# Kernel tuning notes

Measured on AMD Instinct MI355X. Metric: run time of the kernel, lower is better.

## Reference

```python
import jax, jax.numpy as jnp
import numpy as np

B, S, I, H = 32, 1024, 1024, 1024

def setup_inputs() -> dict:
    key = jax.random.key(0)
    k1, k2, k3, k4, k5 = jax.random.split(key, 5)
    bound = 1.0 / np.sqrt(I + H)  # nn.Linear default init scale
    return {
        "x": jax.random.normal(k1, (B, S, I), dtype=jnp.float32),
        "h0": jax.random.normal(k2, (1, B, H), dtype=jnp.float32),
        "c0": jax.random.normal(k3, (1, B, H), dtype=jnp.float32),
        "W": jax.random.uniform(k4, (H, I + H), dtype=jnp.float32, minval=-bound, maxval=bound),
        "b": jax.random.uniform(k5, (H,), dtype=jnp.float32, minval=-bound, maxval=bound),
    }

def reference(x, h0, c0, W, b):
    # NOTE: original torch module applies the SAME linear layer to h_x for all
    # four gates, so f_t == i_t == o_t == sigmoid(z) and C_tilde = tanh(z).
    # Concat order is (h, x): W[:, :H] multiplies h, W[:, H:] multiplies x.
    Wh = W[:, :x.shape[-1] if False else h0.shape[-1]]  # [H, H]
    Wx = W[:, h0.shape[-1]:]                            # [H, I]
    h_init = h0[0]  # [B, H]
    c_init = c0[0]  # [B, H]
    # Precompute the input contribution for all timesteps in one big GEMM.
    xz = jnp.einsum('bsi,hi->sbh', x, Wx) + b  # [S, B, H]

    def step(carry, xz_t):
        h, c = carry
        z = h @ Wh.T + xz_t          # [B, H] shared gate pre-activation
        s = jax.nn.sigmoid(z)        # f_t == i_t == o_t
        c_new = s * c + s * jnp.tanh(z)
        h_new = s * jnp.tanh(c_new)
        return (h_new, c_new), h_new

    (hn, cn), outs = jax.lax.scan(step, (h_init, c_init), xz)
    out = jnp.swapaxes(outs, 0, 1)  # [B, S, H]
    return out, hn[None], cn[None]
```

## Files before the change

### kernel.cpp

```cpp
#include <hip/hip_runtime.h>

#define B_ 32
#define S_ 1024
#define H_ 1024
#define NWG 64
#define EXN (32 * 1024)

typedef float f32x4 __attribute__((ext_vector_type(4)));
typedef short bf16x8 __attribute__((ext_vector_type(8)));
typedef unsigned short u16;

__device__ __forceinline__ short f2bf(float f) {
  union { float f; unsigned u; } v; v.f = f;
  unsigned r = v.u + 0x7FFFu + ((v.u >> 16) & 1u);
  return (short)(r >> 16);
}

__device__ __forceinline__ bf16x8 ldg_coh_b8(const u16* p) {
  bf16x8 r;
  asm volatile("global_load_dwordx4 %0, %1, off sc0 sc1"
               : "=v"(r) : "v"(p) : "memory");
  return r;
}
__device__ __forceinline__ void stg_coh_u16(u16* p, u16 v) {
  asm volatile("global_store_short %0, %1, off sc0 sc1"
               :: "v"(p), "v"(v) : "memory");
}

__global__ __launch_bounds__(256) void xz_gemm(
    const float* __restrict__ X, const float* __restrict__ W,
    const float* __restrict__ bias, float* __restrict__ C) {
  __shared__ short As[128][40];
  __shared__ short Bs[128][40];
  const int tid  = threadIdx.x;
  const int lane = tid & 63, wave = tid >> 6;
  const int m0 = blockIdx.y * 128, n0 = blockIdx.x * 128;
  const int wm = (wave >> 1) * 64, wn = (wave & 1) * 64;
  const int jl = lane & 15, kq = lane >> 4;
  const int sr = tid >> 2, skg = (tid & 3) * 8;

  f32x4 zero4 = {0.f, 0.f, 0.f, 0.f};
  f32x4 acc[4][4];
  #pragma unroll
  for (int mi = 0; mi < 4; ++mi)
    #pragma unroll
    for (int ni = 0; ni < 4; ++ni) acc[mi][ni] = zero4;

  for (int k0 = 0; k0 < 1024; k0 += 32) {
    #pragma unroll
    for (int rr = 0; rr < 2; ++rr) {
      int row = sr + rr * 64;
      const float* pa = X + (size_t)(m0 + row) * 1024 + k0 + skg;
      f32x4 a0 = *(const f32x4*)pa;
      f32x4 a1 = *(const f32x4*)(pa + 4);
      bf16x8 pk;
      #pragma unroll
      for (int e = 0; e < 4; ++e) { pk[e] = f2bf(a0[e]); pk[e + 4] = f2bf(a1[e]); }
      *(bf16x8*)&As[row][skg] = pk;
      const float* pb = W + (size_t)(n0 + row) * 2048 + 1024 + k0 + skg;
      f32x4 b0 = *(const f32x4*)pb;
      f32x4 b1 = *(const f32x4*)(pb + 4);
      bf16x8 qk;
      #pragma unroll
      for (int e = 0; e < 4; ++e) { qk[e] = f2bf(b0[e]); qk[e + 4] = f2bf(b1[e]); }
      *(bf16x8*)&Bs[row][skg] = qk;
    }
    __syncthreads();
    bf16x8 af[4], bfv[4];
    #pragma unroll
    for (int mi = 0; mi < 4; ++mi) af[mi] = *(const bf16x8*)&As[wm + mi * 16 + jl][kq * 8];
    #pragma unroll
    for (int ni = 0; ni < 4; ++ni) bfv[ni] = *(const bf16x8*)&Bs[wn + ni * 16 + jl][kq * 8];
    #pragma unroll
    for (int mi = 0; mi < 4; ++mi)
      #pragma unroll
      for (int ni = 0; ni < 4; ++ni)
        acc[mi][ni] = __builtin_amdgcn_mfma_f32_16x16x32_bf16(af[mi], bfv[ni], acc[mi][ni], 0, 0, 0);
    __syncthreads();
  }
  #pragma unroll
  for (int ni = 0; ni < 4; ++ni) {
    int col = n0 + wn + ni * 16 + jl;
    float bv = bias[col];
    #pragma unroll
    for (int mi = 0; mi < 4; ++mi) {
      int rbase = m0 + wm + mi * 16 + kq * 4;
      #pragma unroll
      for (int r = 0; r < 4; ++r)
        C[(size_t)(rbase + r) * 1024 + col] = acc[mi][ni][r] + bv;
    }
  }
}

__global__ __launch_bounds__(512) void lstm_rec(
    const float* __restrict__ W, const float* __restrict__ h0,
    const float* __restrict__ c0, float* __restrict__ out,
    u16* __restrict__ exch, unsigned* __restrict__ flags) {
  __shared__ short Whs[32 * 1024];
  __shared__ float zred[8][2][64][4];
  const int tid  = threadIdx.x;
  const int lane = tid & 63, wave = tid >> 6;
  const int jl = lane & 15, kq = lane >> 4;
  const int bg = blockIdx.x >> 5;
  const int cg = blockIdx.x & 31;

  {
    int j  = tid >> 4;
    int g0 = (tid & 15) * 8;
    const float* wrow = W + (size_t)(cg * 32 + j) * 2048;
    #pragma unroll
    for (int g = 0; g < 8; ++g) {
      int grp = g0 + g;
      const float* p = wrow + grp * 8;
      f32x4 a0 = *(const f32x4*)p;
      f32x4 a1 = *(const f32x4*)(p + 4);
      bf16x8 pk;
      #pragma unroll
      for (int e = 0; e < 4; ++e) { pk[e] = f2bf(a0[e]); pk[e + 4] = f2bf(a1[e]); }
      *(bf16x8*)&Whs[(j * 128 + (grp ^ (j & 7))) * 8] = pk;
    }
  }

  const int bp   = tid >> 5;
  const int cp   = tid & 31;
  const int b    = bg * 16 + bp;
  const int col  = cg * 32 + cp;
  float cst  = c0[b * 1024 + col];
  float hcur = 0.f;
  stg_coh_u16(exch + b * 1024 + col, (u16)f2bf(h0[b * 1024 + col]));
  __syncthreads();
  if (tid == 0)
    __hip_atomic_store(&flags[blockIdx.x * 16], 1u,
                       __ATOMIC_RELAXED, __HIP_MEMORY_SCOPE_AGENT);

  bf16x8 bfr[2][4];
  #pragma unroll
  for (int ct = 0; ct < 2; ++ct)
    #pragma unroll
    for (int kk = 0; kk < 4; ++kk) {
      int j2  = ct * 16 + jl;
      int grp = wave * 16 + kk * 4 + kq;
      bfr[ct][kk] = *(const bf16x8*)&Whs[(j2 * 128 + (grp ^ (j2 & 7))) * 8];
    }

  const int ct_o = cp >> 4;
  const int j16  = cp & 15;
  const int lred = ((bp >> 2) << 4) | j16;
  const int rred = bp & 3;
  const size_t obase = (size_t)b * (S_ * H_) + col;
  const u16* aptr = exch + (size_t)(bg * 16 + jl) * 1024 + wave * 128 + kq * 8;

  for (int t = 0; t < S_; ++t) {
    float xz = out[obase + (size_t)t * H_];

    if (lane < 4) {
      const unsigned* fp = flags + ((bg << 5) | (wave * 4 + lane)) * 16;
      while (__hip_atomic_load(fp, __ATOMIC_RELAXED, __HIP_MEMORY_SCOPE_AGENT)
             < (unsigned)(t + 1))
        __builtin_amdgcn_s_sleep(1);
    }

    const u16* src = aptr + (t & 1) * EXN;
    bf16x8 afr[4];
    #pragma unroll
    for (int kk = 0; kk < 4; ++kk) afr[kk] = ldg_coh_b8(src + kk * 32);
    asm volatile("s_waitcnt vmcnt(0)" ::: "memory");
    __builtin_amdgcn_sched_barrier(0);

    #pragma unroll
    for (int ct = 0; ct < 2; ++ct) {
      f32x4 pacc = {0.f, 0.f, 0.f, 0.f};
      #pragma unroll
      for (int kk = 0; kk < 4; ++kk)
        pacc = __builtin_amdgcn_mfma_f32_16x16x32_bf16(afr[kk], bfr[ct][kk], pacc, 0, 0, 0);
      *(f32x4*)&zred[wave][ct][lane][0] = pacc;
    }
    __syncthreads();

    float z = xz;
    #pragma unroll
    for (int w = 0; w < 8; ++w) z += zred[w][ct_o][lred][rred];
    float sg  = 1.f / (1.f + __expf(-z));
    float e2z = __expf(2.f * z);
    float tz  = 1.f - 2.f / (e2z + 1.f);
    cst  = sg * (cst + tz);
    float e2c = __expf(2.f * cst);
    float tc  = 1.f - 2.f / (e2c + 1.f);
    hcur = sg * tc;
    stg_coh_u16(exch + ((t + 1) & 1) * EXN + b * 1024 + col, (u16)f2bf(hcur));
    __syncthreads();
    if (tid == 0)
      __hip_atomic_store(&flags[blockIdx.x * 16], (unsigned)(t + 2),
                         __ATOMIC_RELAXED, __HIP_MEMORY_SCOPE_AGENT);
    out[obase + (size_t)t * H_] = hcur;
  }

  const size_t OFS = (size_t)B_ * S_ * H_;
  out[OFS + b * 1024 + col] = hcur;
  out[OFS + (size_t)B_ * H_ + b * 1024 + col] = cst;
}

extern "C" void kernel_launch(void* const* d_in, const int* in_sizes, int n_in,
                              void* d_out, int out_size, void* d_ws, size_t ws_size,
                              hipStream_t stream) {
  const float* x    = (const float*)d_in[0];
  const float* h0   = (const float*)d_in[1];
  const float* c0   = (const float*)d_in[2];
  const float* W    = (const float*)d_in[3];
  const float* bias = (const float*)d_in[4];
  float* out = (float*)d_out;

  u16* exch = (u16*)d_ws;
  unsigned* flags = (unsigned*)((char*)d_ws + 2 * EXN * sizeof(u16));
  hipMemsetAsync(flags, 0, NWG * 16 * sizeof(unsigned), stream);

  xz_gemm<<<dim3(8, 256), 256, 0, stream>>>(x, W, bias, out);
  lstm_rec<<<dim3(NWG), 512, 0, stream>>>(W, h0, c0, out, exch, flags);
}
```

Measured before the change: 2.635 ms.

## Replace flag-based inter-block sync with tagged h exchange words

New measurement: 3.437 ms. 30.4% more time.

```diff
diff --git a/kernel.cpp b/kernel.cpp
--- a/kernel.cpp
+++ b/kernel.cpp
@@ -4,10 +4,11 @@
 #define S_ 1024
 #define H_ 1024
 #define NWG 64
-#define EXN (32 * 1024)
+#define EXN32 (32 * 1024)
 
 typedef float f32x4 __attribute__((ext_vector_type(4)));
 typedef short bf16x8 __attribute__((ext_vector_type(8)));
+typedef unsigned int u32x4 __attribute__((ext_vector_type(4)));
 typedef unsigned short u16;
 
 __device__ __forceinline__ short f2bf(float f) {
@@ -16,15 +17,18 @@
   return (short)(r >> 16);
 }
 
-__device__ __forceinline__ bf16x8 ldg_coh_b8(const u16* p) {
-  bf16x8 r;
-  asm volatile("global_load_dwordx4 %0, %1, off sc0 sc1"
-               : "=v"(r) : "v"(p) : "memory");
-  return r;
-}
-__device__ __forceinline__ void stg_coh_u16(u16* p, u16 v) {
-  asm volatile("global_store_short %0, %1, off sc0 sc1"
+__device__ __forceinline__ void stg_coh_u32(unsigned* p, unsigned v) {
+  asm volatile("global_store_dword %0, %1, off sc0 sc1"
                :: "v"(p), "v"(v) : "memory");
+}
+
+__device__ __forceinline__ bf16x8 mk_frag(u32x4 lo, u32x4 hi) {
+  union { unsigned u[4]; bf16x8 v; } c;
+  c.u[0] = (lo[0] >> 16) | (lo[1] & 0xffff0000u);
+  c.u[1] = (lo[2] >> 16) | (lo[3] & 0xffff0000u);
+  c.u[2] = (hi[0] >> 16) | (hi[1] & 0xffff0000u);
+  c.u[3] = (hi[2] >> 16) | (hi[3] & 0xffff0000u);
+  return c.v;
 }
 
 __global__ __launch_bounds__(256) void xz_gemm(
@@ -95,9 +99,9 @@
 __global__ __launch_bounds__(512) void lstm_rec(
     const float* __restrict__ W, const float* __restrict__ h0,
     const float* __restrict__ c0, float* __restrict__ out,
-    u16* __restrict__ exch, unsigned* __restrict__ flags) {
+    unsigned* __restrict__ exch) {
   __shared__ short Whs[32 * 1024];
-  __shared__ float zred[8][2][64][4];
+  __shared__ float zred[2][8][2][64][5];
   const int tid  = threadIdx.x;
   const int lane = tid & 63, wave = tid >> 6;
   const int jl = lane & 15, kq = lane >> 4;
@@ -121,17 +125,15 @@
     }
   }
 
-  const int bp   = tid >> 5;
-  const int cp   = tid & 31;
-  const int b    = bg * 16 + bp;
-  const int col  = cg * 32 + cp;
+  const int bp  = tid >> 5;
+  const int cp  = tid & 31;
+  const int b   = bg * 16 + bp;
+  const int col = cg * 32 + cp;
   float cst  = c0[b * 1024 + col];
   float hcur = 0.f;
-  stg_coh_u16(exch + b * 1024 + col, (u16)f2bf(h0[b * 1024 + col]));
+  stg_coh_u32(exch + b * 1024 + col,
+              ((unsigned)(u16)f2bf(h0[b * 1024 + col]) << 16) | 1u);
   __syncthreads();
-  if (tid == 0)
-    __hip_atomic_store(&flags[blockIdx.x * 16], 1u,
-                       __ATOMIC_RELAXED, __HIP_MEMORY_SCOPE_AGENT);
 
   bf16x8 bfr[2][4];
   #pragma unroll
@@ -148,38 +150,62 @@
   const int lred = ((bp >> 2) << 4) | j16;
   const int rred = bp & 3;
   const size_t obase = (size_t)b * (S_ * H_) + col;
-  const u16* aptr = exch + (size_t)(bg * 16 + jl) * 1024 + wave * 128 + kq * 8;
+  const unsigned* aptr = exch + (size_t)(bg * 16 + jl) * 1024 + wave * 128 + kq * 8;
+
+  float xz = out[obase];
 
   for (int t = 0; t < S_; ++t) {
-    float xz = out[obase + (size_t)t * H_];
-
-    if (lane < 4) {
-      const unsigned* fp = flags + ((bg << 5) | (wave * 4 + lane)) * 16;
-      while (__hip_atomic_load(fp, __ATOMIC_RELAXED, __HIP_MEMORY_SCOPE_AGENT)
-             < (unsigned)(t + 1))
-        __builtin_amdgcn_s_sleep(1);
-    }
-
-    const u16* src = aptr + (t & 1) * EXN;
+    const unsigned* srcb = aptr + (size_t)(t & 1) * EXN32;
+    const unsigned etag  = (unsigned)(t + 1);
+
+    u32x4 L0, L1, L2, L3, L4, L5, L6, L7;
+#define LDC(dst, off) asm volatile( \
+    "global_load_dwordx4 %0, %1, off offset:" off " sc0 sc1" \
+    : "=v"(dst) : "v"(srcb) : "memory")
+    for (;;) {
+      LDC(L0, "0");   LDC(L1, "16");
+      LDC(L2, "128"); LDC(L3, "144");
+      LDC(L4, "256"); LDC(L5, "272");
+      LDC(L6, "384"); LDC(L7, "400");
+      asm volatile("s_waitcnt vmcnt(0)" ::: "memory");
+      __builtin_amdgcn_sched_barrier(0);
+      unsigned acc;
+      acc  = (L0[0] ^ etag) | (L0[1] ^ etag) | (L0[2] ^ etag) | (L0[3] ^ etag);
+      acc |= (L1[0] ^ etag) | (L1[1] ^ etag) | (L1[2] ^ etag) | (L1[3] ^ etag);
+      acc |= (L2[0] ^ etag) | (L2[1] ^ etag) | (L2[2] ^ etag) | (L2[3] ^ etag);
+      acc |= (L3[0] ^ etag) | (L3[1] ^ etag) | (L3[2] ^ etag) | (L3[3] ^ etag);
+      acc |= (L4[0] ^ etag) | (L4[1] ^ etag) | (L4[2] ^ etag) | (L4[3] ^ etag);
+      acc |= (L5[0] ^ etag) | (L5[1] ^ etag) | (L5[2] ^ etag) | (L5[3] ^ etag);
+      acc |= (L6[0] ^ etag) | (L6[1] ^ etag) | (L6[2] ^ etag) | (L6[3] ^ etag);
+      acc |= (L7[0] ^ etag) | (L7[1] ^ etag) | (L7[2] ^ etag) | (L7[3] ^ etag);
+      if (__all((acc & 0xffffu) == 0u)) break;
+    }
+#undef LDC
+
     bf16x8 afr[4];
-    #pragma unroll
-    for (int kk = 0; kk < 4; ++kk) afr[kk] = ldg_coh_b8(src + kk * 32);
-    asm volatile("s_waitcnt vmcnt(0)" ::: "memory");
-    __builtin_amdgcn_sched_barrier(0);
-
+    afr[0] = mk_frag(L0, L1);
+    afr[1] = mk_frag(L2, L3);
+    afr[2] = mk_frag(L4, L5);
+    afr[3] = mk_frag(L6, L7);
     #pragma unroll
     for (int ct = 0; ct < 2; ++ct) {
       f32x4 pacc = {0.f, 0.f, 0.f, 0.f};
       #pragma unroll
       for (int kk = 0; kk < 4; ++kk)
         pacc = __builtin_amdgcn_mfma_f32_16x16x32_bf16(afr[kk], bfr[ct][kk], pacc, 0, 0, 0);
-      *(f32x4*)&zred[wave][ct][lane][0] = pacc;
-    }
+      #pragma unroll
+      for (int r = 0; r < 4; ++r)
+        zred[t & 1][wave][ct][lane][r] = pacc[r];
+    }
+
+    const size_t nxi = obase + (size_t)(t + 1 < S_ ? t + 1 : t) * H_;
+    float xz_next = out[nxi];
+
     __syncthreads();
 
     float z = xz;
     #pragma unroll
-    for (int w = 0; w < 8; ++w) z += zred[w][ct_o][lred][rred];
+    for (int w = 0; w < 8; ++w) z += zred[t & 1][w][ct_o][lred][rred];
     float sg  = 1.f / (1.f + __expf(-z));
     float e2z = __expf(2.f * z);
     float tz  = 1.f - 2.f / (e2z + 1.f);
@@ -187,12 +213,10 @@
     float e2c = __expf(2.f * cst);
     float tc  = 1.f - 2.f / (e2c + 1.f);
     hcur = sg * tc;
-    stg_coh_u16(exch + ((t + 1) & 1) * EXN + b * 1024 + col, (u16)f2bf(hcur));
-    __syncthreads();
-    if (tid == 0)
-      __hip_atomic_store(&flags[blockIdx.x * 16], (unsigned)(t + 2),
-                         __ATOMIC_RELAXED, __HIP_MEMORY_SCOPE_AGENT);
+    stg_coh_u32(exch + (size_t)((t + 1) & 1) * EXN32 + b * 1024 + col,
+                ((unsigned)(u16)f2bf(hcur) << 16) | (unsigned)(t + 2));
     out[obase + (size_t)t * H_] = hcur;
+    xz = xz_next;
   }
 
   const size_t OFS = (size_t)B_ * S_ * H_;
@@ -210,10 +234,9 @@
   const float* bias = (const float*)d_in[4];
   float* out = (float*)d_out;
 
-  u16* exch = (u16*)d_ws;
-  unsigned* flags = (unsigned*)((char*)d_ws + 2 * EXN * sizeof(u16));
-  hipMemsetAsync(flags, 0, NWG * 16 * sizeof(unsigned), stream);
+  unsigned* exch = (unsigned*)d_ws;
+  hipMemsetAsync(exch, 0, 2 * EXN32 * sizeof(unsigned), stream);
 
   xz_gemm<<<dim3(8, 256), 256, 0, stream>>>(x, W, bias, out);
-  lstm_rec<<<dim3(NWG), 512, 0, stream>>>(W, h0, c0, out, exch, flags);
-}
+  lstm_rec<<<dim3(NWG), 512, 0, stream>>>(W, h0, c0, out, exch);
+}
```

## Restructure recurrent kernel to single-wave workgroups holding Wh slice in registers

Applied to the files above, without the earlier changes.

Result: slower. 4.239 ms (+60.9%).

```diff
diff --git a/kernel.cpp b/kernel.cpp
--- a/kernel.cpp
+++ b/kernel.cpp
@@ -3,7 +3,6 @@
 #define B_ 32
 #define S_ 1024
 #define H_ 1024
-#define NWG 64
 #define EXN (32 * 1024)
 
 typedef float f32x4 __attribute__((ext_vector_type(4)));
@@ -16,14 +15,12 @@
   return (short)(r >> 16);
 }
 
-__device__ __forceinline__ bf16x8 ldg_coh_b8(const u16* p) {
-  bf16x8 r;
-  asm volatile("global_load_dwordx4 %0, %1, off sc0 sc1"
-               : "=v"(r) : "v"(p) : "memory");
-  return r;
-}
 __device__ __forceinline__ void stg_coh_u16(u16* p, u16 v) {
   asm volatile("global_store_short %0, %1, off sc0 sc1"
+               :: "v"(p), "v"(v) : "memory");
+}
+__device__ __forceinline__ void stg_coh_u32(unsigned* p, unsigned v) {
+  asm volatile("global_store_dword %0, %1, off sc0 sc1"
                :: "v"(p), "v"(v) : "memory");
 }
 
@@ -92,112 +89,114 @@
   }
 }
 
-__global__ __launch_bounds__(512) void lstm_rec(
+__global__ __launch_bounds__(64) void lstm_rec(
     const float* __restrict__ W, const float* __restrict__ h0,
     const float* __restrict__ c0, float* __restrict__ out,
     u16* __restrict__ exch, unsigned* __restrict__ flags) {
-  __shared__ short Whs[32 * 1024];
-  __shared__ float zred[8][2][64][4];
-  const int tid  = threadIdx.x;
-  const int lane = tid & 63, wave = tid >> 6;
-  const int jl = lane & 15, kq = lane >> 4;
-  const int bg = blockIdx.x >> 5;
-  const int cg = blockIdx.x & 31;
-
+  const int lane = threadIdx.x & 63;
+  const int wg   = blockIdx.x;
+  const int bt   = wg >> 6;
+  const int ct   = wg & 63;
+  const int jl   = lane & 15, kq = lane >> 4;
+
+  bf16x8 Bf[32];
   {
-    int j  = tid >> 4;
-    int g0 = (tid & 15) * 8;
-    const float* wrow = W + (size_t)(cg * 32 + j) * 2048;
-    #pragma unroll
-    for (int g = 0; g < 8; ++g) {
-      int grp = g0 + g;
-      const float* p = wrow + grp * 8;
+    const float* wrow = W + (size_t)(ct * 16 + jl) * 2048;
+    #pragma unroll
+    for (int kk = 0; kk < 32; ++kk) {
+      const float* p = wrow + kk * 32 + kq * 8;
       f32x4 a0 = *(const f32x4*)p;
       f32x4 a1 = *(const f32x4*)(p + 4);
       bf16x8 pk;
       #pragma unroll
       for (int e = 0; e < 4; ++e) { pk[e] = f2bf(a0[e]); pk[e + 4] = f2bf(a1[e]); }
-      *(bf16x8*)&Whs[(j * 128 + (grp ^ (j & 7))) * 8] = pk;
-    }
-  }
-
-  const int bp   = tid >> 5;
-  const int cp   = tid & 31;
-  const int b    = bg * 16 + bp;
-  const int col  = cg * 32 + cp;
-  float cst  = c0[b * 1024 + col];
-  float hcur = 0.f;
-  stg_coh_u16(exch + b * 1024 + col, (u16)f2bf(h0[b * 1024 + col]));
-  __syncthreads();
-  if (tid == 0)
-    __hip_atomic_store(&flags[blockIdx.x * 16], 1u,
-                       __ATOMIC_RELAXED, __HIP_MEMORY_SCOPE_AGENT);
-
-  bf16x8 bfr[2][4];
-  #pragma unroll
-  for (int ct = 0; ct < 2; ++ct)
-    #pragma unroll
-    for (int kk = 0; kk < 4; ++kk) {
-      int j2  = ct * 16 + jl;
-      int grp = wave * 16 + kk * 4 + kq;
-      bfr[ct][kk] = *(const bf16x8*)&Whs[(j2 * 128 + (grp ^ (j2 & 7))) * 8];
-    }
-
-  const int ct_o = cp >> 4;
-  const int j16  = cp & 15;
-  const int lred = ((bp >> 2) << 4) | j16;
-  const int rred = bp & 3;
-  const size_t obase = (size_t)b * (S_ * H_) + col;
-  const u16* aptr = exch + (size_t)(bg * 16 + jl) * 1024 + wave * 128 + kq * 8;
+      Bf[kk] = pk;
+    }
+  }
+
+  const int b0  = bt * 16 + kq * 4;
+  const int col = ct * 16 + jl;
+  float c[4], h[4];
+  #pragma unroll
+  for (int r = 0; r < 4; ++r) {
+    c[r] = c0[(b0 + r) * 1024 + col];
+    h[r] = h0[(b0 + r) * 1024 + col];
+  }
+  #pragma unroll
+  for (int r = 0; r < 4; ++r)
+    stg_coh_u16(exch + (b0 + r) * 1024 + col, (u16)f2bf(h[r]));
+  asm volatile("s_waitcnt vmcnt(0)" ::: "memory");
+  unsigned* myflag = flags + wg;
+  if (lane == 0) stg_coh_u32(myflag, 1u);
+
+  const u16* aB = exch + (size_t)(bt * 16 + jl) * 1024 + kq * 8;
+  const unsigned* fptr = flags + (bt << 6) + lane;
 
   for (int t = 0; t < S_; ++t) {
-    float xz = out[obase + (size_t)t * H_];
-
-    if (lane < 4) {
-      const unsigned* fp = flags + ((bg << 5) | (wave * 4 + lane)) * 16;
-      while (__hip_atomic_load(fp, __ATOMIC_RELAXED, __HIP_MEMORY_SCOPE_AGENT)
-             < (unsigned)(t + 1))
-        __builtin_amdgcn_s_sleep(1);
-    }
-
-    const u16* src = aptr + (t & 1) * EXN;
-    bf16x8 afr[4];
-    #pragma unroll
-    for (int kk = 0; kk < 4; ++kk) afr[kk] = ldg_coh_b8(src + kk * 32);
+    float xz[4];
+    #pragma unroll
+    for (int r = 0; r < 4; ++r)
+      xz[r] = out[((size_t)(b0 + r) * S_ + t) * H_ + col];
+
+    unsigned fv;
+    for (;;) {
+      asm volatile("global_load_dword %0, %1, off sc0 sc1"
+                   : "=v"(fv) : "v"(fptr) : "memory");
+      asm volatile("s_waitcnt vmcnt(0)" ::: "memory");
+      if (__all(fv > (unsigned)t)) break;
+      __builtin_amdgcn_s_sleep(1);
+    }
+    __builtin_amdgcn_sched_barrier(0);
+
+    const u16* src = aB + (size_t)(t & 1) * EXN;
+    bf16x8 A[32];
+#define LDA(K, OFF) asm volatile( \
+    "global_load_dwordx4 %0, %1, off offset:" OFF " sc0 sc1" \
+    : "=v"(A[K]) : "v"(src) : "memory")
+    LDA(0, "0");     LDA(1, "64");    LDA(2, "128");   LDA(3, "192");
+    LDA(4, "256");   LDA(5, "320");   LDA(6, "384");   LDA(7, "448");
+    LDA(8, "512");   LDA(9, "576");   LDA(10, "640");  LDA(11, "704");
+    LDA(12, "768");  LDA(13, "832");  LDA(14, "896");  LDA(15, "960");
+    LDA(16, "1024"); LDA(17, "1088"); LDA(18, "1152"); LDA(19, "1216");
+    LDA(20, "1280"); LDA(21, "1344"); LDA(22, "1408"); LDA(23, "1472");
+    LDA(24, "1536"); LDA(25, "1600"); LDA(26, "1664"); LDA(27, "1728");
+    LDA(28, "1792"); LDA(29, "1856"); LDA(30, "1920"); LDA(31, "1984");
+#undef LDA
     asm volatile("s_waitcnt vmcnt(0)" ::: "memory");
     __builtin_amdgcn_sched_barrier(0);
 
-    #pragma unroll
-    for (int ct = 0; ct < 2; ++ct) {
-      f32x4 pacc = {0.f, 0.f, 0.f, 0.f};
-      #pragma unroll
-      for (int kk = 0; kk < 4; ++kk)
-        pacc = __builtin_amdgcn_mfma_f32_16x16x32_bf16(afr[kk], bfr[ct][kk], pacc, 0, 0, 0);
-      *(f32x4*)&zred[wave][ct][lane][0] = pacc;
-    }
-    __syncthreads();
-
-    float z = xz;
-    #pragma unroll
-    for (int w = 0; w < 8; ++w) z += zred[w][ct_o][lred][rred];
-    float sg  = 1.f / (1.f + __expf(-z));
-    float e2z = __expf(2.f * z);
-    float tz  = 1.f - 2.f / (e2z + 1.f);
-    cst  = sg * (cst + tz);
-    float e2c = __expf(2.f * cst);
-    float tc  = 1.f - 2.f / (e2c + 1.f);
-    hcur = sg * tc;
-    stg_coh_u16(exch + ((t + 1) & 1) * EXN + b * 1024 + col, (u16)f2bf(hcur));
-    __syncthreads();
-    if (tid == 0)
-      __hip_atomic_store(&flags[blockIdx.x * 16], (unsigned)(t + 2),
-                         __ATOMIC_RELAXED, __HIP_MEMORY_SCOPE_AGENT);
-    out[obase + (size_t)t * H_] = hcur;
+    f32x4 acc[4];
+    #pragma unroll
+    for (int a = 0; a < 4; ++a) acc[a] = (f32x4){0.f, 0.f, 0.f, 0.f};
+    #pragma unroll
+    for (int kk = 0; kk < 32; ++kk)
+      acc[kk & 3] = __builtin_amdgcn_mfma_f32_16x16x32_bf16(A[kk], Bf[kk], acc[kk & 3], 0, 0, 0);
+
+    u16* dst = exch + (size_t)((t + 1) & 1) * EXN;
+    #pragma unroll
+    for (int r = 0; r < 4; ++r) {
+      float z  = xz[r] + (acc[0][r] + acc[1][r]) + (acc[2][r] + acc[3][r]);
+      float u  = __expf(-z);
+      float u2 = u * u;
+      float sg = __builtin_amdgcn_rcpf(1.f + u);
+      float tz = (1.f - u2) * __builtin_amdgcn_rcpf(1.f + u2);
+      c[r] = sg * (c[r] + tz);
+      float v  = __expf(-2.f * c[r]);
+      float tc = (1.f - v) * __builtin_amdgcn_rcpf(1.f + v);
+      h[r] = sg * tc;
+      out[((size_t)(b0 + r) * S_ + t) * H_ + col] = h[r];
+      stg_coh_u16(dst + (b0 + r) * 1024 + col, (u16)f2bf(h[r]));
+    }
+    asm volatile("s_waitcnt vmcnt(0)" ::: "memory");
+    if (lane == 0) stg_coh_u32(myflag, (unsigned)(t + 2));
   }
 
   const size_t OFS = (size_t)B_ * S_ * H_;
-  out[OFS + b * 1024 + col] = hcur;
-  out[OFS + (size_t)B_ * H_ + b * 1024 + col] = cst;
+  #pragma unroll
+  for (int r = 0; r < 4; ++r) {
+    out[OFS + (b0 + r) * 1024 + col] = h[r];
+    out[OFS + (size_t)B_ * H_ + (b0 + r) * 1024 + col] = c[r];
+  }
 }
 
 extern "C" void kernel_launch(void* const* d_in, const int* in_sizes, int n_in,
@@ -212,8 +211,8 @@
 
   u16* exch = (u16*)d_ws;
   unsigned* flags = (unsigned*)((char*)d_ws + 2 * EXN * sizeof(u16));
-  hipMemsetAsync(flags, 0, NWG * 16 * sizeof(unsigned), stream);
+  hipMemsetAsync(flags, 0, 128 * sizeof(unsigned), stream);
 
   xz_gemm<<<dim3(8, 256), 256, 0, stream>>>(x, W, bias, out);
-  lstm_rec<<<dim3(NWG), 512, 0, stream>>>(W, h0, c0, out, exch, flags);
-}
+  lstm_rec<<<dim3(128), 64, 0, stream>>>(W, h0, c0, out, exch, flags);
+}
```

## Replace second block barrier with LDS counter publish and lighter coherence flags

Applied to the files above, without the earlier changes.

Measured after the change: 3.017 ms. 1.14x slower.

```diff
diff --git a/kernel.cpp b/kernel.cpp
--- a/kernel.cpp
+++ b/kernel.cpp
@@ -16,15 +16,11 @@
   return (short)(r >> 16);
 }
 
-__device__ __forceinline__ bf16x8 ldg_coh_b8(const u16* p) {
-  bf16x8 r;
-  asm volatile("global_load_dwordx4 %0, %1, off sc0 sc1"
-               : "=v"(r) : "v"(p) : "memory");
-  return r;
-}
 __device__ __forceinline__ void stg_coh_u16(u16* p, u16 v) {
-  asm volatile("global_store_short %0, %1, off sc0 sc1"
-               :: "v"(p), "v"(v) : "memory");
+  asm volatile("global_store_short %0, %1, off sc1" :: "v"(p), "v"(v) : "memory");
+}
+__device__ __forceinline__ void stg_coh_u32(unsigned* p, unsigned v) {
+  asm volatile("global_store_dword %0, %1, off sc1" :: "v"(p), "v"(v) : "memory");
 }
 
 __global__ __launch_bounds__(256) void xz_gemm(
@@ -97,12 +93,15 @@
     const float* __restrict__ c0, float* __restrict__ out,
     u16* __restrict__ exch, unsigned* __restrict__ flags) {
   __shared__ short Whs[32 * 1024];
-  __shared__ float zred[8][2][64][4];
+  __shared__ float zred[2][8][2][64][5];
+  __shared__ unsigned pubcnt[2];
   const int tid  = threadIdx.x;
   const int lane = tid & 63, wave = tid >> 6;
   const int jl = lane & 15, kq = lane >> 4;
   const int bg = blockIdx.x >> 5;
   const int cg = blockIdx.x & 31;
+
+  if (tid < 2) pubcnt[tid] = 0u;
 
   {
     int j  = tid >> 4;
@@ -121,17 +120,16 @@
     }
   }
 
-  const int bp   = tid >> 5;
-  const int cp   = tid & 31;
-  const int b    = bg * 16 + bp;
-  const int col  = cg * 32 + cp;
+  const int bp  = tid >> 5;
+  const int cp  = tid & 31;
+  const int b   = bg * 16 + bp;
+  const int col = cg * 32 + cp;
   float cst  = c0[b * 1024 + col];
   float hcur = 0.f;
   stg_coh_u16(exch + b * 1024 + col, (u16)f2bf(h0[b * 1024 + col]));
   __syncthreads();
   if (tid == 0)
-    __hip_atomic_store(&flags[blockIdx.x * 16], 1u,
-                       __ATOMIC_RELAXED, __HIP_MEMORY_SCOPE_AGENT);
+    stg_coh_u32(flags + blockIdx.x * 16, 1u);
 
   bf16x8 bfr[2][4];
   #pragma unroll
@@ -149,21 +147,33 @@
   const int rred = bp & 3;
   const size_t obase = (size_t)b * (S_ * H_) + col;
   const u16* aptr = exch + (size_t)(bg * 16 + jl) * 1024 + wave * 128 + kq * 8;
+  unsigned* myflag = flags + blockIdx.x * 16;
+  const unsigned* fptr = flags + (((bg << 5) | (wave * 4 + (lane & 3))) * 16);
+
+  float xz = out[obase];
 
   for (int t = 0; t < S_; ++t) {
-    float xz = out[obase + (size_t)t * H_];
+    const int p = t & 1;
 
     if (lane < 4) {
-      const unsigned* fp = flags + ((bg << 5) | (wave * 4 + lane)) * 16;
-      while (__hip_atomic_load(fp, __ATOMIC_RELAXED, __HIP_MEMORY_SCOPE_AGENT)
-             < (unsigned)(t + 1))
-        __builtin_amdgcn_s_sleep(1);
-    }
-
-    const u16* src = aptr + (t & 1) * EXN;
+      unsigned fv;
+      for (;;) {
+        asm volatile("global_load_dword %0, %1, off sc1"
+                     : "=v"(fv) : "v"(fptr) : "memory");
+        asm volatile("s_waitcnt vmcnt(0)" ::: "memory");
+        if (__all(fv > (unsigned)t)) break;
+      }
+    }
+    __builtin_amdgcn_sched_barrier(0);
+
+    const u16* src = aptr + (size_t)p * EXN;
     bf16x8 afr[4];
-    #pragma unroll
-    for (int kk = 0; kk < 4; ++kk) afr[kk] = ldg_coh_b8(src + kk * 32);
+#define LDA(K, OFF) asm volatile( \
+    "global_load_dwordx4 %0, %1, off offset:" OFF " sc1" \
+    : "=v"(afr[K]) : "v"(src) : "memory")
+    LDA(0, "0"); LDA(1, "64"); LDA(2, "128"); LDA(3, "192");
+#undef LDA
+    float xz_next = out[obase + (size_t)(t + 1 < S_ ? t + 1 : t) * H_];
     asm volatile("s_waitcnt vmcnt(0)" ::: "memory");
     __builtin_amdgcn_sched_barrier(0);
 
@@ -173,26 +183,37 @@
       #pragma unroll
       for (int kk = 0; kk < 4; ++kk)
         pacc = __builtin_amdgcn_mfma_f32_16x16x32_bf16(afr[kk], bfr[ct][kk], pacc, 0, 0, 0);
-      *(f32x4*)&zred[wave][ct][lane][0] = pacc;
-    }
+      #pragma unroll
+      for (int r = 0; r < 4; ++r)
+        zred[p][wave][ct][lane][r] = pacc[r];
+    }
+
     __syncthreads();
 
     float z = xz;
     #pragma unroll
-    for (int w = 0; w < 8; ++w) z += zred[w][ct_o][lred][rred];
-    float sg  = 1.f / (1.f + __expf(-z));
-    float e2z = __expf(2.f * z);
-    float tz  = 1.f - 2.f / (e2z + 1.f);
+    for (int w = 0; w < 8; ++w) z += zred[p][w][ct_o][lred][rred];
+    float u  = __expf(-z);
+    float u2 = u * u;
+    float sg = __builtin_amdgcn_rcpf(1.f + u);
+    float tz = (1.f - u2) * __builtin_amdgcn_rcpf(1.f + u2);
     cst  = sg * (cst + tz);
-    float e2c = __expf(2.f * cst);
-    float tc  = 1.f - 2.f / (e2c + 1.f);
+    float v  = __expf(-2.f * cst);
+    float tc = (1.f - v) * __builtin_amdgcn_rcpf(1.f + v);
     hcur = sg * tc;
-    stg_coh_u16(exch + ((t + 1) & 1) * EXN + b * 1024 + col, (u16)f2bf(hcur));
-    __syncthreads();
-    if (tid == 0)
-      __hip_atomic_store(&flags[blockIdx.x * 16], (unsigned)(t + 2),
-                         __ATOMIC_RELAXED, __HIP_MEMORY_SCOPE_AGENT);
+    stg_coh_u16(exch + (size_t)(p ^ 1) * EXN + b * 1024 + col, (u16)f2bf(hcur));
+    asm volatile("s_waitcnt vmcnt(0)" ::: "memory");
+    if (lane == 0) {
+      unsigned c8 = __hip_atomic_fetch_add(&pubcnt[p], 1u, __ATOMIC_RELAXED,
+                                           __HIP_MEMORY_SCOPE_WORKGROUP);
+      if (c8 == 7u) {
+        stg_coh_u32(myflag, (unsigned)(t + 2));
+        __hip_atomic_store(&pubcnt[p], 0u, __ATOMIC_RELAXED,
+                           __HIP_MEMORY_SCOPE_WORKGROUP);
+      }
+    }
     out[obase + (size_t)t * H_] = hcur;
+    xz = xz_next;
   }
 
   const size_t OFS = (size_t)B_ * S_ * H_;
```
